# Kernel optimization log

Measured on AMD Instinct MI355X. Metric: run time of the kernel, lower is better.

Reference implementation:

```python
import jax, jax.numpy as jnp
import numpy as np

# ---- fixed architecture constants (from init_kwargs) ----
N_WALL, N_ROOF, N_WINDOW = 4, 1, 2
N_RC = N_WALL + N_ROOF
HID = 32
ENC_LEN = 48
DT = 900.0
R_OPAQUE, C_OPAQUE = 10.0, 1.0e5
R_TRANS = 2.0
DIRECT_COEF, ABS_WALL_COEF, ABS_ROOF_COEF = 0.5, 0.5, 0.5
C_ZONE = 1.0e5
B, T = 2048, 1440


def setup_inputs() -> dict:
    key = jax.random.key(0)
    k0, k1, k2 = jax.random.split(key, 3)
    input_X = jax.random.normal(k0, (B, T, 7), dtype=jnp.float32)
    # EnvelopeRC deterministic inits
    rc_R_inv = jnp.concatenate([
        1.0 / (10.0 + 1.0 * jnp.arange(N_WALL, dtype=jnp.float32)),
        1.0 / (20.0 + 2.0 * jnp.arange(N_ROOF, dtype=jnp.float32))])
    rc_C_inv = jnp.concatenate([
        1.0 / (80.0 + 10.0 * jnp.arange(N_WALL, dtype=jnp.float32)),
        1.0 / (60.0 + 10.0 * jnp.arange(N_ROOF, dtype=jnp.float32))])
    window_R_inv = 1.0 / (1.0 + 0.1 * jnp.arange(N_WINDOW, dtype=jnp.float32))
    # Internal MLP: xavier_uniform with gain 0.1, zero bias
    lim1 = 0.1 * np.sqrt(6.0 / (2 + HID))
    int_W1 = jax.random.uniform(k1, (HID, 2), jnp.float32, -lim1, lim1)
    int_b1 = jnp.zeros((HID,), jnp.float32)
    lim2 = 0.1 * np.sqrt(6.0 / (HID + 1))
    int_W2 = jax.random.uniform(k2, (1, HID), jnp.float32, -lim2, lim2)
    int_b2 = jnp.zeros((1,), jnp.float32)
    return {
        'input_X': input_X,
        'rc_R_inv': rc_R_inv, 'rc_C_inv': rc_C_inv, 'window_R_inv': window_R_inv,
        'hvac_gain': jnp.float32(0.1),
        'int_W1': int_W1, 'int_b1': int_b1, 'int_W2': int_W2, 'int_b2': int_b2,
        'int_gain': jnp.float32(0.1),
        'direct_gain': jnp.float32(0.1), 'abs_wall': jnp.float32(0.1), 'abs_roof': jnp.float32(0.1),
        'zone_C_inv': jnp.float32(1.0 / 10000.0),
    }


def _forward(input_X, rc_R_inv, rc_C_inv, window_R_inv, hvac_gain,
             int_W1, int_b1, int_W2, int_b2, int_gain,
             direct_gain, abs_wall, abs_roof, zone_C_inv):
    sp = jax.nn.softplus
    Bn, Tn = input_X.shape[0], input_X.shape[1]
    tz_gt  = input_X[:, :, 0]   # [B,T]
    t_amb  = input_X[:, :, 1]
    sol    = input_X[:, :, 2]
    int_x  = input_X[:, :, 3:6]
    hvac_x = input_X[:, :, 6]

    # Internal MLP (state-free -> vectorized over time)
    h1  = jax.nn.relu(jnp.einsum('bti,hi->bth', int_x[:, :, :2], int_W1) + int_b1)
    sch = jax.nn.sigmoid(jnp.einsum('bth,oh->bto', h1, int_W2) + int_b2)[:, :, 0] + int_x[:, :, 2]
    q_int  = sp(int_gain) * 0.1 * sch          # [B,T]
    q_hvac = sp(hvac_gain) * 0.1 * hvac_x      # [B,T]

    # Bounded RC parameters
    r_inv   = sp(rc_R_inv) * (1.0 / R_OPAQUE)  # [n_rc]
    c_inv   = sp(rc_C_inv) * (1.0 / C_OPAQUE)  # [n_rc]
    win_rsum = jnp.sum(sp(window_R_inv)) * (1.0 / R_TRANS)
    abs_rc  = jnp.where(jnp.arange(N_RC) < N_WALL,
                        sp(abs_wall) * ABS_WALL_COEF,
                        sp(abs_roof) * ABS_ROOF_COEF)   # [n_rc]
    q_dir   = sp(direct_gain) * DIRECT_COEF * sol       # [B,T]
    cz_inv  = sp(zone_C_inv) * (1.0 / C_ZONE)

    # Initial state: Tmid_i = 0.7*Tzone0 + 0.3*Tamb0
    Tz0   = tz_gt[:, 0]                                      # [B]
    Tmid0 = jnp.broadcast_to((0.7 * Tz0 + 0.3 * t_amb[:, 0])[:, None], (Bn, N_RC))

    # Teacher forcing during encoder window: carry GT zone temp while t+1 < enc_len
    tz_gt_next = jnp.concatenate([tz_gt[:, 1:], tz_gt[:, -1:]], axis=1)  # [B,T]
    use_gt = (jnp.arange(Tn) + 1) < ENC_LEN                              # [T]

    xs = (t_amb.T, sol.T, q_dir.T, q_int.T, q_hvac.T, tz_gt_next.T, use_gt)

    def step(carry, x):
        Tz, Tmid = carry                      # [B], [B,n_rc]
        ta, so, qd, qi, qh, gt_next, ug = x
        q_in  = (ta[:, None] - Tmid) * r_inv
        q_out = (Tmid - Tz[:, None]) * r_inv
        dTmid = (q_in - q_out + so[:, None] * abs_rc) * c_inv
        q_env = jnp.sum(q_out, axis=1) + (ta - Tz) * win_rsum
        dTz   = (q_env + qi + qh + qd) * cz_inv
        Tz_new   = Tz + dTz * DT
        Tmid_new = Tmid + dTmid * DT
        Tz_carry = jnp.where(ug, gt_next, Tz_new)
        return (Tz_carry, Tmid_new), Tz_new

    _, tz_seq = jax.lax.scan(step, (Tz0, Tmid0), xs)   # [T,B]
    return jnp.transpose(tz_seq)[:, :, None]           # [B,T,1]


def reference(input_X, rc_R_inv, rc_C_inv, window_R_inv, hvac_gain,
              int_W1, int_b1, int_W2, int_b2, int_gain,
              direct_gain, abs_wall, abs_roof, zone_C_inv):
    return _forward(input_X, rc_R_inv, rc_C_inv, window_R_inv, hvac_gain,
                    int_W1, int_b1, int_W2, int_b2, int_gain,
                    direct_gain, abs_wall, abs_roof, zone_C_inv)
```

## Files before the change

kernel.cpp:

```cpp
#include <hip/hip_runtime.h>
#include <math.h>

#define BATCH 2048
#define TLEN  1440
#define NC    30
#define CL    48

#define E_OFF    0
#define XC_OFF   (E_OFF + NC*6*BATCH)
#define A48_OFF  (XC_OFF + BATCH*NC*6)
#define VCOL_OFF (A48_OFF + 64)
#define PRM_OFF  (VCOL_OFF + 320)
#define WS_FLOATS (PRM_OFF + 32)

__device__ __forceinline__ float sp_precise(float x) { return log1pf(expf(x)); }

__global__ void k0_params(const float* __restrict__ rcR, const float* __restrict__ rcC,
                          const float* __restrict__ winR, const float* __restrict__ hvg,
                          const float* __restrict__ ing, const float* __restrict__ dg,
                          const float* __restrict__ aw, const float* __restrict__ ar,
                          const float* __restrict__ zc, float* __restrict__ ws) {
  __shared__ float A0s[36], Ma[36], Mb[36], M16[36], vbuf[2][8];
  int ln = threadIdx.x;
  float r[5], cc[5];
  #pragma unroll
  for (int j = 0; j < 5; ++j) { r[j] = sp_precise(rcR[j]) * 0.1f; cc[j] = sp_precise(rcC[j]) * 1e-5f; }
  float w    = (sp_precise(winR[0]) + sp_precise(winR[1])) * 0.5f;
  float cz   = sp_precise(zc[0]) * 1e-5f;
  float aW   = sp_precise(aw[0]) * 0.5f, aR = sp_precise(ar[0]) * 0.5f;
  float dtcz = 900.f * cz;
  if (ln == 0) {
    float* prm = ws + PRM_OFF;
    float rsum = 0.f;
    for (int j = 0; j < 5; ++j) {
      float P = 900.f * r[j] * cc[j];
      prm[j]      = P;
      prm[5 + j]  = 1.f - 2.f * P;
      prm[10 + j] = 900.f * cc[j] * ((j < 4) ? aW : aR);
      prm[15 + j] = dtcz * r[j];
      rsum += r[j];
    }
    prm[20] = 1.f - dtcz * (w + rsum);
    prm[21] = dtcz * w;
    prm[22] = dtcz;
    prm[23] = sp_precise(ing[0]) * 0.1f;
    prm[24] = sp_precise(hvg[0]) * 0.1f;
    prm[25] = sp_precise(dg[0])  * 0.5f;
    for (int i = 0; i < 36; ++i) A0s[i] = 0.f;
    A0s[0] = prm[20];
    for (int j = 0; j < 5; ++j) {
      A0s[0 * 6 + 1 + j]       = dtcz * r[j];
      A0s[(1 + j) * 6 + 0]     = prm[j];
      A0s[(1 + j) * 6 + 1 + j] = prm[5 + j];
    }
  }
  __syncthreads();
  int i6 = ln / 6, j6 = ln % 6;
  bool act = ln < 36;
#define MM(DST, L, R) { if (act) { float s = 0.f; \
  for (int m = 0; m < 6; ++m) s = fmaf((L)[i6 * 6 + m], (R)[m * 6 + j6], s); \
  (DST)[ln] = s; } __syncthreads(); }
  MM(Mb, A0s, A0s);
  MM(Ma, Mb, Mb);
  MM(Mb, Ma, Ma);
  MM(Ma, Mb, Mb);
  if (act) M16[ln] = Ma[ln];
  __syncthreads();
  MM(Mb, Ma, Ma);
  MM(Ma, Mb, M16);
  if (act) ws[A48_OFF + ln] = Ma[ln];
  if (ln < 6) vbuf[0][ln] = A0s[ln];
  __syncthreads();
  int cur = 0;
  for (int k = 0; k < CL; ++k) {
    if (ln < 6) {
      ws[VCOL_OFF + ln * CL + k] = vbuf[cur][ln];
      float s = 0.f;
      for (int m = 0; m < 6; ++m) s = fmaf(vbuf[cur][m], A0s[m * 6 + ln], s);
      vbuf[1 - cur][ln] = s;
    }
    __syncthreads();
    cur ^= 1;
  }
}

__global__ __launch_bounds__(256) void k2a_scan(const float* __restrict__ X,
    const float* __restrict__ W1, const float* __restrict__ B1,
    const float* __restrict__ W2, const float* __restrict__ B2,
    float* __restrict__ out, float* __restrict__ ws) {
  int tid = blockIdx.x * 256 + threadIdx.x;
  int c = tid >> 11;
  int b = tid & (BATCH - 1);
  const float* prm = ws + PRM_OFF;
  float P0 = prm[0], P1 = prm[1], P2 = prm[2], P3 = prm[3], P4 = prm[4];
  float M0 = prm[5], M1 = prm[6], M2 = prm[7], M3 = prm[8], M4 = prm[9];
  float Q0 = prm[10], Q1 = prm[11], Q2 = prm[12], Q3 = prm[13], Q4 = prm[14];
  float K0 = prm[15], K1 = prm[16], K2 = prm[17], K3 = prm[18], K4 = prm[19];
  float AZ = prm[20];
  float dtczw = prm[21], dtcz = prm[22], cInt = prm[23], cHv = prm[24], cDir = prm[25];
  const float* xr = X + ((size_t)b * TLEN + (size_t)c * CL) * 7;
  float Tz, T0, T1, T2, T3, T4;
  bool isc0 = (c == 0);
  if (isc0) {
    float tz0 = xr[0], ta0 = xr[1];
    Tz = tz0;
    float tm = fmaf(0.7f, tz0, 0.3f * ta0);
    T0 = T1 = T2 = T3 = T4 = tm;
  } else {
    Tz = 0.f; T0 = T1 = T2 = T3 = T4 = 0.f;
  }
  float* op = out + (size_t)b * TLEN + c * CL;
  float ob0 = 0.f, ob1 = 0.f, ob2 = 0.f, ob3 = 0.f;
  #pragma unroll 4
  for (int k = 0; k < CL; ++k) {
    const float* x = xr + k * 7;
    float ta = x[1], so = x[2], x3 = x[3], x4 = x[4], x5 = x[5], hv = x[6];
    float acc = B2[0];
    #pragma unroll
    for (int h = 0; h < 32; ++h) {
      float z = fmaf(W1[2 * h], x3, fmaf(W1[2 * h + 1], x4, B1[h]));
      acc = fmaf(W2[h], fmaxf(z, 0.f), acc);
    }
    float sch = __frcp_rn(1.f + __expf(-acc)) + x5;
    float q = fmaf(cInt, sch, fmaf(cHv, hv, cDir * so));
    float u = fmaf(dtczw, ta, dtcz * q);
    float d = fmaf(K0, T0, u);
    d = fmaf(K1, T1, d); d = fmaf(K2, T2, d); d = fmaf(K3, T3, d); d = fmaf(K4, T4, d);
    float tzn = fmaf(AZ, Tz, d);
    T0 = fmaf(M0, T0, fmaf(P0, Tz, fmaf(P0, ta, Q0 * so)));
    T1 = fmaf(M1, T1, fmaf(P1, Tz, fmaf(P1, ta, Q1 * so)));
    T2 = fmaf(M2, T2, fmaf(P2, Tz, fmaf(P2, ta, Q2 * so)));
    T3 = fmaf(M3, T3, fmaf(P3, Tz, fmaf(P3, ta, Q3 * so)));
    T4 = fmaf(M4, T4, fmaf(P4, Tz, fmaf(P4, ta, Q4 * so)));
    int ph = k & 3;
    if (ph == 0) ob0 = tzn;
    else if (ph == 1) ob1 = tzn;
    else if (ph == 2) ob2 = tzn;
    else {
      ob3 = tzn;
      ((float4*)op)[k >> 2] = make_float4(ob0, ob1, ob2, ob3);
    }
    float nz = tzn;
    if (isc0 && k < 47) nz = x[7];
    Tz = nz;
  }
  float* e = ws + E_OFF + (size_t)c * 6 * BATCH + b;
  e[0] = Tz;
  e[BATCH] = T0; e[2 * BATCH] = T1; e[3 * BATCH] = T2; e[4 * BATCH] = T3; e[5 * BATCH] = T4;
}

__global__ __launch_bounds__(256) void k2b_combine(float* __restrict__ ws) {
  int b = blockIdx.x * 256 + threadIdx.x;
  __shared__ float A48s[36];
  if (threadIdx.x < 36) A48s[threadIdx.x] = ws[A48_OFF + threadIdx.x];
  __syncthreads();
  const float* e = ws + E_OFF;
  float Xs[6];
  #pragma unroll
  for (int j = 0; j < 6; ++j) Xs[j] = e[j * BATCH + b];
  float* xc = ws + XC_OFF + (size_t)b * NC * 6;
  for (int c = 1; c < NC; ++c) {
    #pragma unroll
    for (int j = 0; j < 6; ++j) xc[c * 6 + j] = Xs[j];
    if (c < NC - 1) {
      float Y[6];
      #pragma unroll
      for (int i = 0; i < 6; ++i) {
        float s = e[((size_t)c * 6 + i) * BATCH + b];
        #pragma unroll
        for (int m = 0; m < 6; ++m) s = fmaf(A48s[i * 6 + m], Xs[m], s);
        Y[i] = s;
      }
      #pragma unroll
      for (int j = 0; j < 6; ++j) Xs[j] = Y[j];
    }
  }
}

__global__ __launch_bounds__(256) void k2c_correct(float* __restrict__ out,
                                                   const float* __restrict__ ws) {
  __shared__ float V[6 * CL];
  for (int i = threadIdx.x; i < 6 * CL; i += 256) V[i] = ws[VCOL_OFF + i];
  __syncthreads();
  int tid = blockIdx.x * 256 + threadIdx.x;
  int b = tid / (TLEN - CL);
  int tt = tid - b * (TLEN - CL);
  int t = tt + CL;
  int c = t / CL;
  int kk = t - c * CL;
  const float* xc = ws + XC_OFF + ((size_t)b * NC + c) * 6;
  float s = out[(size_t)b * TLEN + t];
  #pragma unroll
  for (int j = 0; j < 6; ++j) s = fmaf(V[j * CL + kk], xc[j], s);
  out[(size_t)b * TLEN + t] = s;
}

__global__ void k_fallback(const float* __restrict__ X,
    const float* __restrict__ rcR, const float* __restrict__ rcC,
    const float* __restrict__ winR, const float* __restrict__ hvg,
    const float* __restrict__ W1, const float* __restrict__ B1,
    const float* __restrict__ W2, const float* __restrict__ B2,
    const float* __restrict__ ing, const float* __restrict__ dg,
    const float* __restrict__ aw, const float* __restrict__ ar,
    const float* __restrict__ zc, float* __restrict__ out) {
  int b = blockIdx.x * 64 + threadIdx.x;
  if (b >= BATCH) return;
  float r[5], cc[5], P[5], M[5], Q[5], K[5];
  float rsum = 0.f;
  for (int j = 0; j < 5; ++j) { r[j] = sp_precise(rcR[j]) * 0.1f; cc[j] = sp_precise(rcC[j]) * 1e-5f; rsum += r[j]; }
  float w = (sp_precise(winR[0]) + sp_precise(winR[1])) * 0.5f;
  float cz = sp_precise(zc[0]) * 1e-5f;
  float aW = sp_precise(aw[0]) * 0.5f, aR = sp_precise(ar[0]) * 0.5f;
  float dtcz = 900.f * cz;
  for (int j = 0; j < 5; ++j) {
    P[j] = 900.f * r[j] * cc[j]; M[j] = 1.f - 2.f * P[j];
    Q[j] = 900.f * cc[j] * ((j < 4) ? aW : aR); K[j] = dtcz * r[j];
  }
  float AZ = 1.f - dtcz * (w + rsum), dtczw = dtcz * w;
  float cInt = sp_precise(ing[0]) * 0.1f, cHv = sp_precise(hvg[0]) * 0.1f, cDir = sp_precise(dg[0]) * 0.5f;
  const float* xb = X + (size_t)b * (TLEN * 7);
  float Tz = xb[0];
  float tm = fmaf(0.7f, xb[0], 0.3f * xb[1]);
  float Tm[5] = {tm, tm, tm, tm, tm};
  for (int t = 0; t < TLEN; ++t) {
    const float* x = xb + t * 7;
    float ta = x[1], so = x[2], x3 = x[3], x4 = x[4], x5 = x[5], hv = x[6];
    float acc = B2[0];
    #pragma unroll
    for (int h = 0; h < 32; ++h) {
      float z = fmaf(W1[2 * h], x3, fmaf(W1[2 * h + 1], x4, B1[h]));
      acc = fmaf(W2[h], fmaxf(z, 0.f), acc);
    }
    float sch = __frcp_rn(1.f + __expf(-acc)) + x5;
    float q = fmaf(cInt, sch, fmaf(cHv, hv, cDir * so));
    float u = fmaf(dtczw, ta, dtcz * q);
    float d = u;
    #pragma unroll
    for (int j = 0; j < 5; ++j) d = fmaf(K[j], Tm[j], d);
    float tzn = fmaf(AZ, Tz, d);
    #pragma unroll
    for (int j = 0; j < 5; ++j)
      Tm[j] = fmaf(M[j], Tm[j], fmaf(P[j], Tz, fmaf(P[j], ta, Q[j] * so)));
    out[(size_t)b * TLEN + t] = tzn;
    Tz = (t < 47) ? x[7] : tzn;
  }
}

extern "C" void kernel_launch(void* const* d_in, const int* in_sizes, int n_in,
                              void* d_out, int out_size, void* d_ws, size_t ws_size,
                              hipStream_t stream) {
  const float* X    = (const float*)d_in[0];
  const float* rcR  = (const float*)d_in[1];
  const float* rcC  = (const float*)d_in[2];
  const float* winR = (const float*)d_in[3];
  const float* hvg  = (const float*)d_in[4];
  const float* W1   = (const float*)d_in[5];
  const float* B1   = (const float*)d_in[6];
  const float* W2   = (const float*)d_in[7];
  const float* B2   = (const float*)d_in[8];
  const float* ing  = (const float*)d_in[9];
  const float* dg   = (const float*)d_in[10];
  const float* aw   = (const float*)d_in[11];
  const float* ar   = (const float*)d_in[12];
  const float* zc   = (const float*)d_in[13];
  float* out = (float*)d_out;
  float* ws  = (float*)d_ws;

  if (ws_size >= (size_t)WS_FLOATS * sizeof(float)) {
    k0_params<<<1, 64, 0, stream>>>(rcR, rcC, winR, hvg, ing, dg, aw, ar, zc, ws);
    k2a_scan<<<(BATCH * NC) / 256, 256, 0, stream>>>(X, W1, B1, W2, B2, out, ws);
    k2b_combine<<<BATCH / 256, 256, 0, stream>>>(ws);
    k2c_correct<<<(BATCH * (TLEN - CL)) / 256, 256, 0, stream>>>(out, ws);
  } else {
    k_fallback<<<BATCH / 64, 64, 0, stream>>>(X, rcR, rcC, winR, hvg, W1, B1, W2, B2,
                                              ing, dg, aw, ar, zc, out);
  }
}
```

Before: 223.0 us.

## Split scan into shorter 12-step chunks and store chunk states batch-major

Result: slower. 284.5 us (+27.6%).

```diff
diff --git a/kernel.cpp b/kernel.cpp
--- a/kernel.cpp
+++ b/kernel.cpp
@@ -3,14 +3,16 @@
 
 #define BATCH 2048
 #define TLEN  1440
-#define NC    30
-#define CL    48
+#define CL0   48
+#define CLS   12
+#define NS    116
+#define NCC   117
 
 #define E_OFF    0
-#define XC_OFF   (E_OFF + NC*6*BATCH)
-#define A48_OFF  (XC_OFF + BATCH*NC*6)
-#define VCOL_OFF (A48_OFF + 64)
-#define PRM_OFF  (VCOL_OFF + 320)
+#define XC_OFF   (E_OFF + NCC*6*BATCH)
+#define A12_OFF  (XC_OFF + NCC*6*BATCH)
+#define VCOL_OFF (A12_OFF + 64)
+#define PRM_OFF  (VCOL_OFF + 96)
 #define WS_FLOATS (PRM_OFF + 32)
 
 __device__ __forceinline__ float sp_precise(float x) { return log1pf(expf(x)); }
@@ -20,7 +22,7 @@
                           const float* __restrict__ ing, const float* __restrict__ dg,
                           const float* __restrict__ aw, const float* __restrict__ ar,
                           const float* __restrict__ zc, float* __restrict__ ws) {
-  __shared__ float A0s[36], Ma[36], Mb[36], M16[36], vbuf[2][8];
+  __shared__ float A0s[36], Ma[36], Mb[36], A4s[36], vbuf[2][8];
   int ln = threadIdx.x;
   float r[5], cc[5];
   #pragma unroll
@@ -62,19 +64,17 @@
   (DST)[ln] = s; } __syncthreads(); }
   MM(Mb, A0s, A0s);
   MM(Ma, Mb, Mb);
+  if (act) A4s[ln] = Ma[ln];
+  __syncthreads();
   MM(Mb, Ma, Ma);
-  MM(Ma, Mb, Mb);
-  if (act) M16[ln] = Ma[ln];
-  __syncthreads();
-  MM(Mb, Ma, Ma);
-  MM(Ma, Mb, M16);
-  if (act) ws[A48_OFF + ln] = Ma[ln];
+  MM(Ma, Mb, A4s);
+  if (act) ws[A12_OFF + ln] = Ma[ln];
   if (ln < 6) vbuf[0][ln] = A0s[ln];
   __syncthreads();
   int cur = 0;
-  for (int k = 0; k < CL; ++k) {
+  for (int k = 0; k < CLS; ++k) {
     if (ln < 6) {
-      ws[VCOL_OFF + ln * CL + k] = vbuf[cur][ln];
+      ws[VCOL_OFF + ln * CLS + k] = vbuf[cur][ln];
       float s = 0.f;
       for (int m = 0; m < 6; ++m) s = fmaf(vbuf[cur][m], A0s[m * 6 + ln], s);
       vbuf[1 - cur][ln] = s;
@@ -98,9 +98,11 @@
   float K0 = prm[15], K1 = prm[16], K2 = prm[17], K3 = prm[18], K4 = prm[19];
   float AZ = prm[20];
   float dtczw = prm[21], dtcz = prm[22], cInt = prm[23], cHv = prm[24], cDir = prm[25];
-  const float* xr = X + ((size_t)b * TLEN + (size_t)c * CL) * 7;
+  bool isc0 = (c == 0);
+  int tstart = isc0 ? 0 : CL0 + (c - 1) * CLS;
+  int L = isc0 ? CL0 : CLS;
+  const float* xr = X + ((size_t)b * TLEN + tstart) * 7;
   float Tz, T0, T1, T2, T3, T4;
-  bool isc0 = (c == 0);
   if (isc0) {
     float tz0 = xr[0], ta0 = xr[1];
     Tz = tz0;
@@ -109,10 +111,10 @@
   } else {
     Tz = 0.f; T0 = T1 = T2 = T3 = T4 = 0.f;
   }
-  float* op = out + (size_t)b * TLEN + c * CL;
+  float* op = out + (size_t)b * TLEN + tstart;
   float ob0 = 0.f, ob1 = 0.f, ob2 = 0.f, ob3 = 0.f;
   #pragma unroll 4
-  for (int k = 0; k < CL; ++k) {
+  for (int k = 0; k < L; ++k) {
     const float* x = xr + k * 7;
     float ta = x[1], so = x[2], x3 = x[3], x4 = x[4], x5 = x[5], hv = x[6];
     float acc = B2[0];
@@ -151,24 +153,24 @@
 
 __global__ __launch_bounds__(256) void k2b_combine(float* __restrict__ ws) {
   int b = blockIdx.x * 256 + threadIdx.x;
-  __shared__ float A48s[36];
-  if (threadIdx.x < 36) A48s[threadIdx.x] = ws[A48_OFF + threadIdx.x];
+  __shared__ float A12s[36];
+  if (threadIdx.x < 36) A12s[threadIdx.x] = ws[A12_OFF + threadIdx.x];
   __syncthreads();
   const float* e = ws + E_OFF;
   float Xs[6];
   #pragma unroll
   for (int j = 0; j < 6; ++j) Xs[j] = e[j * BATCH + b];
-  float* xc = ws + XC_OFF + (size_t)b * NC * 6;
-  for (int c = 1; c < NC; ++c) {
-    #pragma unroll
-    for (int j = 0; j < 6; ++j) xc[c * 6 + j] = Xs[j];
-    if (c < NC - 1) {
+  float* xc = ws + XC_OFF;
+  for (int c = 1; c < NCC; ++c) {
+    #pragma unroll
+    for (int j = 0; j < 6; ++j) xc[((size_t)c * 6 + j) * BATCH + b] = Xs[j];
+    if (c < NCC - 1) {
       float Y[6];
       #pragma unroll
       for (int i = 0; i < 6; ++i) {
         float s = e[((size_t)c * 6 + i) * BATCH + b];
         #pragma unroll
-        for (int m = 0; m < 6; ++m) s = fmaf(A48s[i * 6 + m], Xs[m], s);
+        for (int m = 0; m < 6; ++m) s = fmaf(A12s[i * 6 + m], Xs[m], s);
         Y[i] = s;
       }
       #pragma unroll
@@ -179,20 +181,20 @@
 
 __global__ __launch_bounds__(256) void k2c_correct(float* __restrict__ out,
                                                    const float* __restrict__ ws) {
-  __shared__ float V[6 * CL];
-  for (int i = threadIdx.x; i < 6 * CL; i += 256) V[i] = ws[VCOL_OFF + i];
+  __shared__ float V[6 * CLS];
+  for (int i = threadIdx.x; i < 6 * CLS; i += 256) V[i] = ws[VCOL_OFF + i];
   __syncthreads();
   int tid = blockIdx.x * 256 + threadIdx.x;
-  int b = tid / (TLEN - CL);
-  int tt = tid - b * (TLEN - CL);
-  int t = tt + CL;
-  int c = t / CL;
-  int kk = t - c * CL;
-  const float* xc = ws + XC_OFF + ((size_t)b * NC + c) * 6;
-  float s = out[(size_t)b * TLEN + t];
+  int b = tid / (TLEN - CL0);
+  int tt = tid - b * (TLEN - CL0);
+  int c = tt / CLS + 1;
+  int kk = tt - (c - 1) * CLS;
+  const float* xc = ws + XC_OFF;
+  float s = out[(size_t)b * TLEN + CL0 + tt];
   #pragma unroll
-  for (int j = 0; j < 6; ++j) s = fmaf(V[j * CL + kk], xc[j], s);
-  out[(size_t)b * TLEN + t] = s;
+  for (int j = 0; j < 6; ++j)
+    s = fmaf(V[j * CLS + kk], xc[((size_t)c * 6 + j) * BATCH + b], s);
+  out[(size_t)b * TLEN + CL0 + tt] = s;
 }
 
 __global__ void k_fallback(const float* __restrict__ X,
@@ -268,9 +270,9 @@
 
   if (ws_size >= (size_t)WS_FLOATS * sizeof(float)) {
     k0_params<<<1, 64, 0, stream>>>(rcR, rcC, winR, hvg, ing, dg, aw, ar, zc, ws);
-    k2a_scan<<<(BATCH * NC) / 256, 256, 0, stream>>>(X, W1, B1, W2, B2, out, ws);
+    k2a_scan<<<(BATCH * NCC) / 256, 256, 0, stream>>>(X, W1, B1, W2, B2, out, ws);
     k2b_combine<<<BATCH / 256, 256, 0, stream>>>(ws);
-    k2c_correct<<<(BATCH * (TLEN - CL)) / 256, 256, 0, stream>>>(out, ws);
+    k2c_correct<<<(BATCH * (TLEN - CL0)) / 256, 256, 0, stream>>>(out, ws);
   } else {
     k_fallback<<<BATCH / 64, 64, 0, stream>>>(X, rcR, rcC, winR, hvg, W1, B1, W2, B2,
                                               ing, dg, aw, ar, zc, out);
```
